# Optimization experiments

Measured on AMD Instinct MI355X. Metric: run time of the kernel, lower is better.

The kernel has to match this reference:

```python
import jax, jax.numpy as jnp
from jax import lax
import numpy as np

B = 2048; IMG = 28; K = 3; CIN = 1; HC = 32; LC = 16; WID = 64; HID = 64
LIS = IMG - 3 * (K - 1)           # 22: latent image size
FLAT = LIS * LIS * HC             # 15488
BLK = WID * LC                    # 1024: hypernet block size
T1 = 10.0; T0 = 0.0; NSTEP = 20   # fixed-step RK4 replaces adaptive dopri5
VAR = 0.1                         # p_z0 diagonal covariance


def _conv(x, w, b):  # w: [Cout,Cin,k,k], VALID conv, stride 1
    y = lax.conv_general_dilated(x, w, (1, 1), 'VALID',
                                 dimension_numbers=('NCHW', 'OIHW', 'NCHW'))
    return y + b[None, :, None, None]


def _convT(x, w, b):  # w: [Cin,Cout,k,k] (pytorch ConvTranspose2d layout)
    wf = jnp.flip(w, (2, 3)).transpose(1, 0, 2, 3)  # -> OIHW, spatially flipped
    y = lax.conv_general_dilated(x, wf, (1, 1), [(K - 1, K - 1), (K - 1, K - 1)],
                                 dimension_numbers=('NCHW', 'OIHW', 'NCHW'))
    return y + b[None, :, None, None]


def _forward(x, c0w, c0b, c1w, c1b, c2w, c2b, elw, elb, dlw, dlb,
             t0w, t0b, t1w, t1b, t2w, t2b, h1w, h1b, h2w, h2b, h3w, h3b):
    # ---- encoder (dropout in eval = identity) ----
    h = jnp.tanh(_conv(x, c0w, c0b))
    h = jnp.tanh(_conv(h, c1w, c1b))
    h = jnp.tanh(_conv(h, c2w, c2b))
    z1 = h.reshape(h.shape[0], -1) @ elw + elb          # [B, LC]
    # ---- decoder ----
    d = jnp.tanh(z1 @ dlw + dlb)                         # [B, FLAT]
    d = d.reshape(-1, HC, LIS, LIS)
    d = jnp.tanh(_convT(d, t0w, t0b))
    d = jnp.tanh(_convT(d, t1w, t1b))
    recon = _convT(d, t2w, t2b)                          # [B, CIN, 28, 28]

    # ---- CNF vector field with analytic trace ----
    def hyper(t):
        p = jnp.tanh(jnp.reshape(jnp.asarray(t, jnp.float32), (1, 1)) @ h1w + h1b)
        p = jnp.tanh(p @ h2w + h2b)
        p = (p @ h3w + h3b).reshape(-1)
        W = p[:BLK].reshape(WID, LC)
        U = p[BLK:2 * BLK].reshape(WID, LC) * jax.nn.sigmoid(p[2 * BLK:3 * BLK].reshape(WID, LC))
        Bb = p[3 * BLK:]                                 # [WID]
        return W, Bb, U

    def f(t, z):
        W, Bb, U = hyper(t)
        hh = jnp.tanh(jnp.einsum('bd,wd->wb', z, W) + Bb[:, None])   # [WID, B]
        dz = jnp.einsum('wb,wd->bd', hh, U) / WID                     # [B, LC]
        s = jnp.sum(W * U, axis=1)                                    # [WID]: sum_i W_w[i]U_w[i]
        tr = jnp.mean((1.0 - hh * hh) * s[:, None], axis=0)           # [B] analytic trace
        return dz, -tr[:, None]

    dt = (T0 - T1) / NSTEP

    def step(state, i):
        z, lp = state
        t = T1 + i * dt
        k1z, k1l = f(t, z)
        k2z, k2l = f(t + 0.5 * dt, z + 0.5 * dt * k1z)
        k3z, k3l = f(t + 0.5 * dt, z + 0.5 * dt * k2z)
        k4z, k4l = f(t + dt, z + dt * k3z)
        z = z + dt / 6.0 * (k1z + 2 * k2z + 2 * k3z + k4z)
        lp = lp + dt / 6.0 * (k1l + 2 * k2l + 2 * k3l + k4l)
        return (z, lp), None

    lp1 = jnp.zeros((z1.shape[0], 1), z1.dtype)
    (z0, lp0), _ = lax.scan(step, (z1, lp1), jnp.arange(NSTEP, dtype=jnp.float32))

    # MultivariateNormal(0, 0.1*I) log_prob
    logp = -0.5 * (LC * jnp.log(2 * jnp.pi) + LC * jnp.log(VAR) + jnp.sum(z0 * z0, -1) / VAR)
    x_probs = jnp.mean(logp - lp0[:, 0])
    return recon, x_probs


def setup_inputs() -> dict:
    key = jax.random.key(0)
    ks = jax.random.split(key, 16)
    n = jax.random.normal
    s = jnp.float32(0.05)
    z = jnp.zeros
    OUT3 = 3 * BLK + WID
    return {
        'x': n(ks[0], (B, CIN, IMG, IMG), jnp.float32),
        'c0w': n(ks[1], (HC, CIN, K, K)) * s, 'c0b': z((HC,)),
        'c1w': n(ks[2], (HC, HC, K, K)) * s, 'c1b': z((HC,)),
        'c2w': n(ks[3], (HC, HC, K, K)) * s, 'c2b': z((HC,)),
        'elw': n(ks[4], (FLAT, LC)) * s, 'elb': z((LC,)),
        'dlw': n(ks[5], (LC, FLAT)) * s, 'dlb': z((FLAT,)),
        't0w': n(ks[6], (HC, HC, K, K)) * s, 't0b': z((HC,)),
        't1w': n(ks[7], (HC, HC, K, K)) * s, 't1b': z((HC,)),
        't2w': n(ks[8], (HC, CIN, K, K)) * s, 't2b': z((CIN,)),
        'h1w': n(ks[9], (1, HID)) * s, 'h1b': z((HID,)),
        'h2w': n(ks[10], (HID, HID)) * s, 'h2b': z((HID,)),
        'h3w': n(ks[11], (HID, OUT3)) * s, 'h3b': z((OUT3,)),
    }


def reference(x, c0w, c0b, c1w, c1b, c2w, c2b, elw, elb, dlw, dlb,
              t0w, t0b, t1w, t1b, t2w, t2b, h1w, h1b, h2w, h2b, h3w, h3b):
    return _forward(x, c0w, c0b, c1w, c1b, c2w, c2b, elw, elb, dlw, dlb,
                    t0w, t0b, t1w, t1b, t2w, t2b, h1w, h1b, h2w, h2b, h3w, h3b)
```

## Files before the change

### kernel.cpp

```cpp
#include <hip/hip_runtime.h>
#include <math.h>

#define Bsz 2048

using bf16x8 = __attribute__((ext_vector_type(8))) short;
using f32x4  = __attribute__((ext_vector_type(4))) float;

__device__ __forceinline__ float fast_tanh(float x){
    float e = __expf(2.0f * x);
    return 1.0f - 2.0f / (e + 1.0f);
}
__device__ __forceinline__ float fast_sigmoid(float x){
    return 1.0f / (1.0f + __expf(-x));
}
__device__ __forceinline__ unsigned short f2b(float f){
    union { float f; unsigned u; } v; v.f = f;
    unsigned r = v.u + 0x7FFFu + ((v.u >> 16) & 1u);
    return (unsigned short)(r >> 16);
}
__device__ __forceinline__ float b2f(unsigned short s){
    union { unsigned u; float f; } v; v.u = ((unsigned)s) << 16;
    return v.f;
}

__device__ __forceinline__ float stage_t(int sidx){
    int i  = sidx >> 2, st = sidx & 3;
    float t = 10.0f - 0.5f * (float)i;
    if (st == 1 || st == 2) t -= 0.25f;
    else if (st == 3)       t -= 0.5f;
    return t;
}

__global__ void k_prep(const float* __restrict__ c1w, const float* __restrict__ c2w,
                       const float* __restrict__ t0w, const float* __restrict__ t1w,
                       const float* __restrict__ elw, const float* __restrict__ dlw,
                       const float* __restrict__ elb, const float* __restrict__ dlb,
                       const float* __restrict__ t2w,
                       unsigned short* __restrict__ wc1, unsigned short* __restrict__ wc2,
                       unsigned short* __restrict__ wt0, unsigned short* __restrict__ wt1,
                       unsigned short* __restrict__ t2wPk,
                       unsigned short* __restrict__ elwT, unsigned short* __restrict__ dlwT,
                       float* __restrict__ dlbT, float* __restrict__ z1, int full){
    int gsz = gridDim.x * 256;
    for (int i = blockIdx.x*256 + threadIdx.x; i < 9216; i += gsz){
        int ci = i & 31, co = (i >> 5) & 31, s = i >> 10;
        wc1[i] = f2b(c1w[(co*32 + ci)*9 + s]);
        wc2[i] = f2b(c2w[(co*32 + ci)*9 + s]);
        wt0[i] = f2b(t0w[(ci*32 + co)*9 + (8 - s)]);
        wt1[i] = f2b(t1w[(ci*32 + co)*9 + (8 - s)]);
    }
    if (!full) return;
    for (int i = blockIdx.x*256 + threadIdx.x; i < 288; i += gsz){
        int tap = i >> 5, ci = i & 31;
        int r = tap / 3, s = tap - r*3;
        t2wPk[i] = f2b(t2w[ci*9 + (2-r)*3 + (2-s)]);
    }
    for (int i = blockIdx.x*256 + threadIdx.x; i < 32768; i += gsz)
        z1[i] = elb[i & 15];
    for (int i = blockIdx.x*256 + threadIdx.x; i < 15488; i += gsz){
        int pos = i >> 5, ci = i & 31;
        dlbT[i] = dlb[ci*484 + pos];
    }
    for (int i = blockIdx.x*256 + threadIdx.x; i < 247808; i += gsz){
        int l = i / 15488, f2 = i - l*15488;
        int pos = f2 >> 5, ci = f2 & 31;
        elwT[i] = f2b(elw[(ci*484 + pos)*16 + l]);
    }
    for (int i = blockIdx.x*256 + threadIdx.x; i < 247808; i += gsz){
        int f2 = i >> 4, l = i & 15;
        int pos = f2 >> 5, ci = f2 & 31;
        dlwT[i] = f2b(dlw[l*15488 + ci*484 + pos]);
    }
}

__global__ void __launch_bounds__(256)
k_enc01(const float* __restrict__ x, const float* __restrict__ c0w,
        const float* __restrict__ c0b, const unsigned short* __restrict__ wc1,
        const float* __restrict__ c1b, unsigned short* __restrict__ A1,
        int cb){
    __shared__ __align__(16) unsigned short A0L[676*40];
    const int tid = threadIdx.x, b = blockIdx.x;
    const float* xin = x + (size_t)(cb + b)*784;

    for (int pos = tid; pos < 676; pos += 256){
        int y = pos / 26, xx = pos - y*26;
        float v[9];
#pragma unroll
        for (int r = 0; r < 3; r++)
#pragma unroll
            for (int s = 0; s < 3; s++)
                v[r*3+s] = xin[(y+r)*28 + xx + s];
        float acc[32];
#pragma unroll
        for (int co = 0; co < 32; co++) acc[co] = c0b[co];
#pragma unroll
        for (int k = 0; k < 9; k++)
#pragma unroll
            for (int co = 0; co < 32; co++)
                acc[co] += v[k] * c0w[co*9 + k];
        unsigned short* ob = A0L + pos*40;
#pragma unroll
        for (int g = 0; g < 8; g++){
            ushort4 o;
            o.x = f2b(fast_tanh(acc[g*4+0])); o.y = f2b(fast_tanh(acc[g*4+1]));
            o.z = f2b(fast_tanh(acc[g*4+2])); o.w = f2b(fast_tanh(acc[g*4+3]));
            *(ushort4*)(ob + g*4) = o;
        }
    }
    __syncthreads();

    const int wave = tid >> 6, lane = tid & 63;
    const int q = lane >> 4, nn = lane & 15;
    bf16x8 af[2][9];
#pragma unroll
    for (int mt = 0; mt < 2; mt++)
#pragma unroll
        for (int s = 0; s < 9; s++)
            af[mt][s] = *(const bf16x8*)(wc1 + s*1024 + (mt*16 + nn)*32 + q*8);
    float4 bc0 = *(const float4*)(c1b + q*4);
    float4 bc1 = *(const float4*)(c1b + 16 + q*4);
    unsigned short* outb = A1 + (size_t)b*25088;

    for (int t = wave; t < 36; t += 4){
        int pos = t*16 + nn;
        int oy = pos / 24, ox = pos - oy*24;
        const unsigned short* ib = A0L + (oy*26 + ox)*40 + q*8;
        f32x4 acc0 = {0.f,0.f,0.f,0.f}, acc1 = {0.f,0.f,0.f,0.f};
#pragma unroll
        for (int r = 0; r < 3; r++){
            bf16x8 b0 = *(const bf16x8*)(ib + (r*26 + 0)*40);
            bf16x8 b1 = *(const bf16x8*)(ib + (r*26 + 1)*40);
            bf16x8 b2 = *(const bf16x8*)(ib + (r*26 + 2)*40);
            acc0 = __builtin_amdgcn_mfma_f32_16x16x32_bf16(af[0][r*3+0], b0, acc0, 0,0,0);
            acc1 = __builtin_amdgcn_mfma_f32_16x16x32_bf16(af[1][r*3+0], b0, acc1, 0,0,0);
            acc0 = __builtin_amdgcn_mfma_f32_16x16x32_bf16(af[0][r*3+1], b1, acc0, 0,0,0);
            acc1 = __builtin_amdgcn_mfma_f32_16x16x32_bf16(af[1][r*3+1], b1, acc1, 0,0,0);
            acc0 = __builtin_amdgcn_mfma_f32_16x16x32_bf16(af[0][r*3+2], b2, acc0, 0,0,0);
            acc1 = __builtin_amdgcn_mfma_f32_16x16x32_bf16(af[1][r*3+2], b2, acc1, 0,0,0);
        }
        int opix = oy*24 + ox;
        ushort4 o0, o1;
        o0.x = f2b(fast_tanh(acc0[0] + bc0.x)); o0.y = f2b(fast_tanh(acc0[1] + bc0.y));
        o0.z = f2b(fast_tanh(acc0[2] + bc0.z)); o0.w = f2b(fast_tanh(acc0[3] + bc0.w));
        o1.x = f2b(fast_tanh(acc1[0] + bc1.x)); o1.y = f2b(fast_tanh(acc1[1] + bc1.y));
        o1.z = f2b(fast_tanh(acc1[2] + bc1.z)); o1.w = f2b(fast_tanh(acc1[3] + bc1.w));
        *(ushort4*)(outb + opix*32 + q*4)      = o0;
        *(ushort4*)(outb + opix*32 + 16 + q*4) = o1;
    }
}

template<int IL, int OL, int OW, int OOFF, int INS, int OUTS>
__global__ void __launch_bounds__(256)
k_convM(const unsigned short* __restrict__ in, const unsigned short* __restrict__ wg,
        const float* __restrict__ bias, unsigned short* __restrict__ out, int CH){
    constexpr int N  = OL * OL;
    constexpr int NT = (N + 15) / 16;
    const int tid = threadIdx.x;
    const int wave = tid >> 6, lane = tid & 63;
    const int q = lane >> 4, nn = lane & 15;
    const int nw = gridDim.x * 4;

    bf16x8 af[2][9];
#pragma unroll
    for (int mt = 0; mt < 2; mt++)
#pragma unroll
        for (int s = 0; s < 9; s++)
            af[mt][s] = *(const bf16x8*)(wg + s*1024 + (mt*16 + nn)*32 + q*8);
    float4 bc0 = *(const float4*)(bias + q*4);
    float4 bc1 = *(const float4*)(bias + 16 + q*4);

    for (int t = blockIdx.x*4 + wave; t < CH*NT; t += nw){
        int img = t / NT, tt = t - img*NT;
        const unsigned short* inb = in + (size_t)img * INS;
        unsigned short* outb = out + (size_t)img * OUTS;
        int pos = tt*16 + nn;
        int pc  = pos < N ? pos : N - 1;
        int oy = pc / OL, ox = pc - oy*OL;
        const unsigned short* ib = inb + (oy*IL + ox)*32 + q*8;
        f32x4 acc0 = {0.f,0.f,0.f,0.f}, acc1 = {0.f,0.f,0.f,0.f};
#pragma unroll
        for (int r = 0; r < 3; r++){
            bf16x8 b0 = *(const bf16x8*)(ib + (r*IL + 0)*32);
            bf16x8 b1 = *(const bf16x8*)(ib + (r*IL + 1)*32);
            bf16x8 b2 = *(const bf16x8*)(ib + (r*IL + 2)*32);
            acc0 = __builtin_amdgcn_mfma_f32_16x16x32_bf16(af[0][r*3+0], b0, acc0, 0,0,0);
            acc1 = __builtin_amdgcn_mfma_f32_16x16x32_bf16(af[1][r*3+0], b0, acc1, 0,0,0);
            acc0 = __builtin_amdgcn_mfma_f32_16x16x32_bf16(af[0][r*3+1], b1, acc0, 0,0,0);
            acc1 = __builtin_amdgcn_mfma_f32_16x16x32_bf16(af[1][r*3+1], b1, acc1, 0,0,0);
            acc0 = __builtin_amdgcn_mfma_f32_16x16x32_bf16(af[0][r*3+2], b2, acc0, 0,0,0);
            acc1 = __builtin_amdgcn_mfma_f32_16x16x32_bf16(af[1][r*3+2], b2, acc1, 0,0,0);
        }
        if (pos < N){
            int opix = oy*OW + ox + OOFF;
            ushort4 o0, o1;
            o0.x = f2b(fast_tanh(acc0[0] + bc0.x)); o0.y = f2b(fast_tanh(acc0[1] + bc0.y));
            o0.z = f2b(fast_tanh(acc0[2] + bc0.z)); o0.w = f2b(fast_tanh(acc0[3] + bc0.w));
            o1.x = f2b(fast_tanh(acc1[0] + bc1.x)); o1.y = f2b(fast_tanh(acc1[1] + bc1.y));
            o1.z = f2b(fast_tanh(acc1[2] + bc1.z)); o1.w = f2b(fast_tanh(acc1[3] + bc1.w));
            *(ushort4*)(outb + opix*32 + q*4)      = o0;
            *(ushort4*)(outb + opix*32 + 16 + q*4) = o1;
        }
    }
}

__global__ void __launch_bounds__(256)
k_encg(const unsigned short* __restrict__ A2, const unsigned short* __restrict__ elwT,
       float* __restrict__ z1, int cb, int CH){
    int wave = threadIdx.x >> 6, lane = threadIdx.x & 63;
    int q = lane >> 4, nn = lane & 15;
    int imgb = blockIdx.x*16;
    const unsigned short* ap = A2 + (size_t)(imgb + nn)*15488 + q*8;
    const unsigned short* bp = elwT + (size_t)nn*15488 + q*8;
    f32x4 acc = {0.f,0.f,0.f,0.f};
    int s0 = blockIdx.y*121;
#pragma unroll 2
    for (int s = s0 + wave; s < s0 + 121; s += 4){
        bf16x8 a = *(const bf16x8*)(ap + s*32);
        bf16x8 b = *(const bf16x8*)(bp + s*32);
        acc = __builtin_amdgcn_mfma_f32_16x16x32_bf16(a, b, acc, 0,0,0);
    }
    float* zp = z1 + (size_t)(cb + imgb)*16;
#pragma unroll
    for (int i = 0; i < 4; i++)
        atomicAdd(zp + (q*4 + i)*16 + nn, acc[i]);
}

__global__ void __launch_bounds__(256)
k_decgM(const float* __restrict__ z1, const unsigned short* __restrict__ dlwT,
        const float* __restrict__ dlbT, unsigned short* __restrict__ D0c, int cb){
    __shared__ float zb[16*17];
    const int tid = threadIdx.x;
    const int wave = tid >> 6, lane = tid & 63;
    const int q = lane >> 4, n = lane & 15;
    const int imgb = blockIdx.y*16;
    zb[(tid >> 4)*17 + (tid & 15)] = z1[(size_t)(cb + imgb + (tid >> 4))*16 + (tid & 15)];
    __syncthreads();

    bf16x8 zf;
    if (q < 2){
        unsigned short tmp[8];
#pragma unroll
        for (int j = 0; j < 8; j++) tmp[j] = f2b(zb[n*17 + q*8 + j]);
        zf = *(bf16x8*)tmp;
    } else {
        bf16x8 zz = {0,0,0,0,0,0,0,0}; zf = zz;
    }

#pragma unroll
    for (int ii = 0; ii < 4; ii++){
        int mt = blockIdx.x*16 + wave*4 + ii;
        if (mt >= 968) break;
        int mb = mt*16;
        bf16x8 afr;
        if (q < 2) afr = *(const bf16x8*)(dlwT + (size_t)(mb + n)*16 + q*8);
        else { bf16x8 zz = {0,0,0,0,0,0,0,0}; afr = zz; }
        f32x4 acc = {0.f,0.f,0.f,0.f};
        acc = __builtin_amdgcn_mfma_f32_16x16x32_bf16(afr, zf, acc, 0,0,0);
        float4 bias = *(const float4*)(dlbT + mb + q*4);
        ushort4 o;
        o.x = f2b(fast_tanh(acc[0] + bias.x));
        o.y = f2b(fast_tanh(acc[1] + bias.y));
        o.z = f2b(fast_tanh(acc[2] + bias.z));
        o.w = f2b(fast_tanh(acc[3] + bias.w));
        *(ushort4*)(D0c + (size_t)(imgb + n)*15488 + mb + q*4) = o;
    }
}

__global__ void __launch_bounds__(256)
k_dect0(const unsigned short* __restrict__ D0c, const unsigned short* __restrict__ wt0,
        const float* __restrict__ t0b, unsigned short* __restrict__ D1){
    __shared__ __align__(16) unsigned short D0L[676*40];
    const int tid = threadIdx.x, b = blockIdx.x;
    unsigned short* d1b = D1 + (size_t)b*25088;

    {
        uint4 zq = {0,0,0,0};
        for (int p = tid; p < 676; p += 256){
            int y = p / 26, xx = p - y*26;
            if (y < 2 || y >= 24 || xx < 2 || xx >= 24){
                uint4* pt = (uint4*)(D0L + p*40);
                pt[0] = zq; pt[1] = zq; pt[2] = zq; pt[3] = zq;
            }
        }
        for (int p = tid; p < 784; p += 256){
            int y = p / 28, xx = p - y*28;
            if (y < 2 || y >= 26 || xx < 2 || xx >= 26){
                uint4* pt = (uint4*)(d1b + p*32);
                pt[0] = zq; pt[1] = zq; pt[2] = zq; pt[3] = zq;
            }
        }
    }
    {
        const uint4* src = (const uint4*)(D0c + (size_t)b*15488);
        for (int c = tid; c < 1936; c += 256){
            uint4 v = src[c];
            int pos = c >> 2, p8 = (c & 3)*8;
            int y = pos / 22, xx = pos - y*22;
            *(uint4*)(D0L + ((y+2)*26 + xx + 2)*40 + p8) = v;
        }
    }
    __syncthreads();

    const int wave = tid >> 6, lane = tid & 63;
    const int q = lane >> 4, nn = lane & 15;
    bf16x8 af[2][9];
#pragma unroll
    for (int mt = 0; mt < 2; mt++)
#pragma unroll
        for (int s = 0; s < 9; s++)
            af[mt][s] = *(const bf16x8*)(wt0 + s*1024 + (mt*16 + nn)*32 + q*8);
    float4 bc0 = *(const float4*)(t0b + q*4);
    float4 bc1 = *(const float4*)(t0b + 16 + q*4);

    for (int t = wave; t < 36; t += 4){
        int pos = t*16 + nn;
        int oy = pos / 24, ox = pos - oy*24;
        const unsigned short* ib = D0L + (oy*26 + ox)*40 + q*8;
        f32x4 acc0 = {0.f,0.f,0.f,0.f}, acc1 = {0.f,0.f,0.f,0.f};
#pragma unroll
        for (int r = 0; r < 3; r++){
            bf16x8 b0 = *(const bf16x8*)(ib + (r*26 + 0)*40);
            bf16x8 b1 = *(const bf16x8*)(ib + (r*26 + 1)*40);
            bf16x8 b2 = *(const bf16x8*)(ib + (r*26 + 2)*40);
            acc0 = __builtin_amdgcn_mfma_f32_16x16x32_bf16(af[0][r*3+0], b0, acc0, 0,0,0);
            acc1 = __builtin_amdgcn_mfma_f32_16x16x32_bf16(af[1][r*3+0], b0, acc1, 0,0,0);
            acc0 = __builtin_amdgcn_mfma_f32_16x16x32_bf16(af[0][r*3+1], b1, acc0, 0,0,0);
            acc1 = __builtin_amdgcn_mfma_f32_16x16x32_bf16(af[1][r*3+1], b1, acc1, 0,0,0);
            acc0 = __builtin_amdgcn_mfma_f32_16x16x32_bf16(af[0][r*3+2], b2, acc0, 0,0,0);
            acc1 = __builtin_amdgcn_mfma_f32_16x16x32_bf16(af[1][r*3+2], b2, acc1, 0,0,0);
        }
        int opix = oy*28 + ox + 58;
        ushort4 o0, o1;
        o0.x = f2b(fast_tanh(acc0[0] + bc0.x)); o0.y = f2b(fast_tanh(acc0[1] + bc0.y));
        o0.z = f2b(fast_tanh(acc0[2] + bc0.z)); o0.w = f2b(fast_tanh(acc0[3] + bc0.w));
        o1.x = f2b(fast_tanh(acc1[0] + bc1.x)); o1.y = f2b(fast_tanh(acc1[1] + bc1.y));
        o1.z = f2b(fast_tanh(acc1[2] + bc1.z)); o1.w = f2b(fast_tanh(acc1[3] + bc1.w));
        *(ushort4*)(d1b + opix*32 + q*4)      = o0;
        *(ushort4*)(d1b + opix*32 + 16 + q*4) = o1;
    }
}

__global__ void __launch_bounds__(256)
k_dect12(const unsigned short* __restrict__ D1, const unsigned short* __restrict__ wt1,
         const float* __restrict__ t1b, const unsigned short* __restrict__ t2wPk,
         const float* __restrict__ t2b, float* __restrict__ out, int cb){
    __shared__ __align__(16) unsigned short D2L[900*40];
    const int tid = threadIdx.x, b = blockIdx.x;
    const unsigned short* d1b = D1 + (size_t)b*25088;
    const int wave = tid >> 6, lane = tid & 63;
    const int q = lane >> 4, nn = lane & 15;

    {
        uint4 zq = {0,0,0,0};
        for (int p = tid; p < 900; p += 256){
            int y = p / 30, xx = p - y*30;
            if (y < 2 || y >= 28 || xx < 2 || xx >= 28){
                uint4* pt = (uint4*)(D2L + p*40);
                pt[0] = zq; pt[1] = zq; pt[2] = zq; pt[3] = zq;
            }
        }
    }
    {
        bf16x8 af[2][9];
#pragma unroll
        for (int mt = 0; mt < 2; mt++)
#pragma unroll
            for (int s = 0; s < 9; s++)
                af[mt][s] = *(const bf16x8*)(wt1 + s*1024 + (mt*16 + nn)*32 + q*8);
        float4 bc0 = *(const float4*)(t1b + q*4);
        float4 bc1 = *(const float4*)(t1b + 16 + q*4);

        for (int t = wave; t < 43; t += 4){
            int pos = t*16 + nn;
            int pc  = pos < 676 ? pos : 675;
            int oy = pc / 26, ox = pc - oy*26;
            const unsigned short* ib = d1b + (oy*28 + ox)*32 + q*8;
            f32x4 acc0 = {0.f,0.f,0.f,0.f}, acc1 = {0.f,0.f,0.f,0.f};
#pragma unroll
            for (int r = 0; r < 3; r++){
                bf16x8 b0 = *(const bf16x8*)(ib + (r*28 + 0)*32);
                bf16x8 b1 = *(const bf16x8*)(ib + (r*28 + 1)*32);
                bf16x8 b2 = *(const bf16x8*)(ib + (r*28 + 2)*32);
                acc0 = __builtin_amdgcn_mfma_f32_16x16x32_bf16(af[0][r*3+0], b0, acc0, 0,0,0);
                acc1 = __builtin_amdgcn_mfma_f32_16x16x32_bf16(af[1][r*3+0], b0, acc1, 0,0,0);
                acc0 = __builtin_amdgcn_mfma_f32_16x16x32_bf16(af[0][r*3+1], b1, acc0, 0,0,0);
                acc1 = __builtin_amdgcn_mfma_f32_16x16x32_bf16(af[1][r*3+1], b1, acc1, 0,0,0);
                acc0 = __builtin_amdgcn_mfma_f32_16x16x32_bf16(af[0][r*3+2], b2, acc0, 0,0,0);
                acc1 = __builtin_amdgcn_mfma_f32_16x16x32_bf16(af[1][r*3+2], b2, acc1, 0,0,0);
            }
            if (pos < 676){
                int opix = (oy + 2)*30 + ox + 2;
                ushort4 o0, o1;
                o0.x = f2b(fast_tanh(acc0[0] + bc0.x)); o0.y = f2b(fast_tanh(acc0[1] + bc0.y));
                o0.z = f2b(fast_tanh(acc0[2] + bc0.z)); o0.w = f2b(fast_tanh(acc0[3] + bc0.w));
                o1.x = f2b(fast_tanh(acc1[0] + bc1.x)); o1.y = f2b(fast_tanh(acc1[1] + bc1.y));
                o1.z = f2b(fast_tanh(acc1[2] + bc1.z)); o1.w = f2b(fast_tanh(acc1[3] + bc1.w));
                *(ushort4*)(D2L + opix*40 + q*4)      = o0;
                *(ushort4*)(D2L + opix*40 + 16 + q*4) = o1;
            }
        }
    }
    __syncthreads();

    {
        bf16x8 wf[9];
#pragma unroll
        for (int tap = 0; tap < 9; tap++)
            wf[tap] = *(const bf16x8*)(t2wPk + tap*32 + q*8);
        float t2b0 = t2b[0];
        for (int t = wave; t < 49; t += 4){
            int p = t*16 + nn;
            int y = p / 28, xx = p - y*28;
            const unsigned short* bbase = D2L + (y*30 + xx)*40 + q*8;
            f32x4 acc = {0.f,0.f,0.f,0.f};
#pragma unroll
            for (int r = 0; r < 3; r++){
                acc = __builtin_amdgcn_mfma_f32_16x16x32_bf16(wf[r*3+0],
                        *(const bf16x8*)(bbase + (r*30 + 0)*40), acc, 0,0,0);
                acc = __builtin_amdgcn_mfma_f32_16x16x32_bf16(wf[r*3+1],
                        *(const bf16x8*)(bbase + (r*30 + 1)*40), acc, 0,0,0);
                acc = __builtin_amdgcn_mfma_f32_16x16x32_bf16(wf[r*3+2],
                        *(const bf16x8*)(bbase + (r*30 + 2)*40), acc, 0,0,0);
            }
            if (q == 0)
                out[(size_t)(cb + b)*784 + p] = acc[0] + t2b0;
        }
    }
}

template<int LOUT, int INW, int OUTW, int OUTOFF>
// ... 209 lines not shown
        ushort4 o0 = {0,0,0,0}, o1 = {0,0,0,0};
        if (q < 2){
            const float* wp = p3 + (c*16 + m)*16 + q*8;
            o0.x = f2b(wp[0]); o0.y = f2b(wp[1]); o0.z = f2b(wp[2]); o0.w = f2b(wp[3]);
            o1.x = f2b(wp[4]); o1.y = f2b(wp[5]); o1.z = f2b(wp[6]); o1.w = f2b(wp[7]);
        }
        *(ushort4*)(gW + tid*8)     = o0;
        *(ushort4*)(gW + tid*8 + 4) = o1;
    }
    if (tid < 128){
        int lane = tid & 63, kb = tid >> 6;
        int q = lane >> 4, d = lane & 15;
        unsigned short uo[8];
#pragma unroll
        for (int j = 0; j < 8; j++){
            int w = kb*32 + q*8 + j;
            float u = p3[1024 + w*16 + d] * fast_sigmoid(p3[2048 + w*16 + d]);
            uo[j] = f2b(u);
        }
        *(ushort4*)(gU + tid*8)     = *(ushort4*)&uo[0];
        *(ushort4*)(gU + tid*8 + 4) = *(ushort4*)&uo[4];
    } else if (tid < 192){
        int w = tid - 128;
        g[1536 + w] = p3[3072 + w];
    } else {
        int w = tid - 192;
        float s = 0.f;
#pragma unroll
        for (int d = 0; d < 16; d++){
            float u = p3[1024 + w*16 + d] * fast_sigmoid(p3[2048 + w*16 + d]);
            s += p3[w*16 + d] * u;
        }
        g[1600 + w] = s;
        sred[w] = s;
    }
    __syncthreads();
    if (tid == 0){
        float st = 0.f;
#pragma unroll
        for (int w = 0; w < 64; w++) st += sred[w];
        g[1664] = st;
    }
}

__global__ void k_hyper(const float* __restrict__ h1w, const float* __restrict__ h1b,
                        const float* __restrict__ h2w, const float* __restrict__ h2b,
                        const float* __restrict__ h3w, const float* __restrict__ h3b,
                        float* __restrict__ hyp){
    int sidx = blockIdx.x;
    float t = stage_t(sidx);
    __shared__ float p1[64], p2[64];
    __shared__ float p3[3136];
    int tid = threadIdx.x;
    if (tid < 64) p1[tid] = fast_tanh(t * h1w[tid] + h1b[tid]);
    __syncthreads();
    if (tid < 64){
        float a = h2b[tid];
#pragma unroll
        for (int k = 0; k < 64; k++) a += p1[k] * h2w[k*64 + tid];
        p2[tid] = fast_tanh(a);
    }
    __syncthreads();
    for (int m = tid; m < 3136; m += 256){
        float a = h3b[m];
#pragma unroll
        for (int k = 0; k < 64; k++) a += p2[k] * h3w[k*3136 + m];
        p3[m] = a;
    }
    __syncthreads();
    float* g = hyp + (size_t)sidx * 2304;
    for (int m = tid; m < 1024; m += 256){
        g[m] = p3[m];
        float u = p3[1024 + m] * fast_sigmoid(p3[2048 + m]);
        g[1024 + (m & 15)*64 + (m >> 4)] = u;
        p3[1024 + m] = u;
    }
    if (tid < 64) g[2048 + tid] = p3[3072 + tid];
    __syncthreads();
    if (tid < 64){
        float s = 0.f;
#pragma unroll
        for (int d = 0; d < 16; d++) s += p3[tid*16 + d] * p3[1024 + tid*16 + d];
        g[2112 + tid] = s;
    }
}

struct PM {
    bf16x8 Wf[4];
    bf16x8 Uf[2];
    float4 Bbf[4];
    float4 sf[4];
    float stot;
};
__device__ __forceinline__ void loadPM(const float* __restrict__ g, int lane, int q, PM& p){
    const unsigned short* gW = (const unsigned short*)g;
    const unsigned short* gU = (const unsigned short*)(g + 1024);
#pragma unroll
    for (int c = 0; c < 4; c++)
        p.Wf[c] = *(const bf16x8*)(gW + (c*64 + lane)*8);
#pragma unroll
    for (int kb = 0; kb < 2; kb++)
        p.Uf[kb] = *(const bf16x8*)(gU + (kb*64 + lane)*8);
#pragma unroll
    for (int c = 0; c < 4; c++){
        p.Bbf[c] = *(const float4*)(g + 1536 + c*16 + q*4);
        p.sf[c]  = *(const float4*)(g + 1600 + c*16 + q*4);
    }
    p.stot = g[1664];
}

__global__ void __launch_bounds__(64)
k_cnfM(const float* __restrict__ z1, const float* __restrict__ hyp,
       float* __restrict__ part){
    __shared__ __align__(16) unsigned short zsb[16*24];
    __shared__ __align__(16) unsigned short hhT[16*72];
    const int lane = threadIdx.x;
    const int q = lane >> 4, d = lane & 15;
    const float dt = -0.5f;

    float z[4], zacc[4], lacc[4], lp[4];
#pragma unroll
    for (int i = 0; i < 4; i++){
        z[i] = z1[(size_t)(blockIdx.x*16 + q*4 + i)*16 + d];
        zacc[i] = 0.f; lacc[i] = 0.f; lp[i] = 0.f;
        zsb[(q*4 + i)*24 + d] = f2b(z[i]);
    }
    PM pm0, pm1;
    loadPM(hyp, lane, q, pm0);

#pragma unroll 2
    for (int sidx = 0; sidx < 80; sidx++){
        PM& cur = (sidx & 1) ? pm1 : pm0;
        PM& nxt = (sidx & 1) ? pm0 : pm1;
        if (sidx < 79) loadPM(hyp + (size_t)(sidx + 1)*2048, lane, q, nxt);

        bf16x8 zb;
        if (q < 2) zb = *(const bf16x8*)(zsb + d*24 + q*8);
        else { bf16x8 zz2 = {0,0,0,0,0,0,0,0}; zb = zz2; }

        f32x4 h0 = {0,0,0,0}, h1 = {0,0,0,0}, h2 = {0,0,0,0}, h3 = {0,0,0,0};
        h0 = __builtin_amdgcn_mfma_f32_16x16x32_bf16(cur.Wf[0], zb, h0, 0,0,0);
        h1 = __builtin_amdgcn_mfma_f32_16x16x32_bf16(cur.Wf[1], zb, h1, 0,0,0);
        h2 = __builtin_amdgcn_mfma_f32_16x16x32_bf16(cur.Wf[2], zb, h2, 0,0,0);
        h3 = __builtin_amdgcn_mfma_f32_16x16x32_bf16(cur.Wf[3], zb, h3, 0,0,0);

        float partial = 0.f;
        f32x4 hc[4] = {h0, h1, h2, h3};
#pragma unroll
        for (int c = 0; c < 4; c++){
            ushort4 o;
            float t0 = fast_tanh(hc[c][0] + cur.Bbf[c].x);
            float t1 = fast_tanh(hc[c][1] + cur.Bbf[c].y);
            float t2 = fast_tanh(hc[c][2] + cur.Bbf[c].z);
            float t3 = fast_tanh(hc[c][3] + cur.Bbf[c].w);
            partial += t0*t0*cur.sf[c].x + t1*t1*cur.sf[c].y
                     + t2*t2*cur.sf[c].z + t3*t3*cur.sf[c].w;
            o.x = f2b(t0); o.y = f2b(t1); o.z = f2b(t2); o.w = f2b(t3);
            *(ushort4*)(hhT + d*72 + c*16 + q*4) = o;
        }
        partial += __shfl_xor(partial, 16);
        partial += __shfl_xor(partial, 32);
        float trFull = (cur.stot - partial) * (1.f/64.f);

        bf16x8 a20 = *(const bf16x8*)(hhT + d*72 + q*8);
        bf16x8 a21 = *(const bf16x8*)(hhT + d*72 + 32 + q*8);
        f32x4 dzac = {0,0,0,0};
        dzac = __builtin_amdgcn_mfma_f32_16x16x32_bf16(a20, cur.Uf[0], dzac, 0,0,0);
        dzac = __builtin_amdgcn_mfma_f32_16x16x32_bf16(a21, cur.Uf[1], dzac, 0,0,0);

        int st = sidx & 3;
        float wgt = (st == 0 || st == 3) ? 1.f : 2.f;
#pragma unroll
        for (int i = 0; i < 4; i++){
            float dz = dzac[i] * (1.f/64.f);
            float dl = -__shfl(trFull, q*4 + i);
            zacc[i] += wgt * dz;
            lacc[i] += wgt * dl;
            float zsv;
            if (st < 3){
                float aa = (st == 2) ? 1.0f : 0.5f;
                zsv = z[i] + aa * dt * dz;
            } else {
                z[i]  += (dt/6.f) * zacc[i];
                lp[i] += (dt/6.f) * lacc[i];
                zsv = z[i];
                zacc[i] = 0.f; lacc[i] = 0.f;
            }
            zsb[(q*4 + i)*24 + d] = f2b(zsv);
        }
    }
    float sq[4];
#pragma unroll
    for (int i = 0; i < 4; i++) sq[i] = z[i]*z[i];
#pragma unroll
    for (int off = 1; off < 16; off <<= 1){
#pragma unroll
        for (int i = 0; i < 4; i++) sq[i] += __shfl_xor(sq[i], off, 16);
    }
    if (d == 0){
#pragma unroll
        for (int i = 0; i < 4; i++){
            float logp = -0.5f * (16.f*1.8378770664093453f
                                 + 16.f*(-2.302585092994046f) + sq[i]*10.f);
            part[blockIdx.x*16 + q*4 + i] = logp - lp[i];
        }
    }
}

struct PF { float4 Wr[4]; float4 Ur[4]; float Bb, sw; };
__device__ __forceinline__ void load_pf(const float* __restrict__ g,
                                        int lane, int q, int d, PF& p){
    const float4* w4 = (const float4*)(g + lane*16);
    p.Wr[0] = w4[0]; p.Wr[1] = w4[1]; p.Wr[2] = w4[2]; p.Wr[3] = w4[3];
    const float4* u4 = (const float4*)(g + 1024 + d*64 + q*16);
    p.Ur[0] = u4[0]; p.Ur[1] = u4[1]; p.Ur[2] = u4[2]; p.Ur[3] = u4[3];
    p.Bb = g[2048 + lane];
    p.sw = g[2112 + lane];
}
__global__ void __launch_bounds__(64)
k_cnf_f(const float* __restrict__ z1, const float* __restrict__ hyp,
        float* __restrict__ part){
    __shared__ __align__(16) float zsl[16];
    __shared__ __align__(16) float hhl[64];
    const int lane = threadIdx.x;
    const int q = lane >> 4, d = lane & 15;
    const float dt = -0.5f;
    float z  = z1[(size_t)blockIdx.x*16 + d];
    float zs = z;
    float lp = 0.f, zacc = 0.f, lacc = 0.f;
    if (lane < 16) zsl[lane] = zs;
    PF cur, nxt;
    load_pf(hyp, lane, q, d, cur);
    for (int sidx = 0; sidx < 80; sidx++){
        __syncthreads();
        if (sidx < 79) load_pf(hyp + (size_t)(sidx + 1)*2304, lane, q, d, nxt);
        const float4* zp = (const float4*)zsl;
        float4 z0 = zp[0], z1v = zp[1], z2 = zp[2], z3 = zp[3];
        float a = cur.Bb;
        a += z0.x*cur.Wr[0].x + z0.y*cur.Wr[0].y + z0.z*cur.Wr[0].z + z0.w*cur.Wr[0].w;
        a += z1v.x*cur.Wr[1].x + z1v.y*cur.Wr[1].y + z1v.z*cur.Wr[1].z + z1v.w*cur.Wr[1].w;
        a += z2.x*cur.Wr[2].x + z2.y*cur.Wr[2].y + z2.z*cur.Wr[2].z + z2.w*cur.Wr[2].w;
        a += z3.x*cur.Wr[3].x + z3.y*cur.Wr[3].y + z3.z*cur.Wr[3].z + z3.w*cur.Wr[3].w;
        float hh = fast_tanh(a);
        float e = (1.f - hh*hh) * cur.sw;
#pragma unroll
        for (int off = 1; off < 64; off <<= 1)
            e += __shfl_xor(e, off);
        hhl[lane] = hh;
        __syncthreads();
        const float4* hp = (const float4*)(hhl + q*16);
        float4 h0 = hp[0], h1 = hp[1], h2 = hp[2], h3 = hp[3];
        float dzp = 0.f;
        dzp += h0.x*cur.Ur[0].x + h0.y*cur.Ur[0].y + h0.z*cur.Ur[0].z + h0.w*cur.Ur[0].w;
        dzp += h1.x*cur.Ur[1].x + h1.y*cur.Ur[1].y + h1.z*cur.Ur[1].z + h1.w*cur.Ur[1].w;
        dzp += h2.x*cur.Ur[2].x + h2.y*cur.Ur[2].y + h2.z*cur.Ur[2].z + h2.w*cur.Ur[2].w;
        dzp += h3.x*cur.Ur[3].x + h3.y*cur.Ur[3].y + h3.z*cur.Ur[3].z + h3.w*cur.Ur[3].w;
        dzp += __shfl_xor(dzp, 16);
        dzp += __shfl_xor(dzp, 32);
        float dz = dzp * (1.f/64.f);
        float dl = -e  * (1.f/64.f);
        int st = sidx & 3;
        float wgt = (st == 0 || st == 3) ? 1.f : 2.f;
        zacc += wgt * dz;
        lacc += wgt * dl;
        if (st < 3){
            float aa = (st == 2) ? 1.0f : 0.5f;
            zs = z + aa * dt * dz;
        } else {
            z  += (dt/6.f) * zacc;
            lp += (dt/6.f) * lacc;
            zs = z;
            zacc = 0.f; lacc = 0.f;
        }
        if (lane < 16) zsl[lane] = zs;
        cur = nxt;
    }
    float sq = z * z;
#pragma unroll
    for (int off = 1; off < 16; off <<= 1) sq += __shfl_xor(sq, off, 16);
    float logp = -0.5f * (16.f*1.8378770664093453f + 16.f*(-2.302585092994046f) + sq*10.f);
    if (lane == 0) part[blockIdx.x] = logp - lp;
}

__global__ void k_final(const float* __restrict__ part, float* __restrict__ out){
    __shared__ float red[256];
    int tid = threadIdx.x;
    float s = 0.f;
#pragma unroll
// ... 1 lines not shown
    red[tid] = s;
    __syncthreads();
    for (int st = 128; st > 0; st >>= 1){
        if (tid < st) red[tid] += red[tid + st];
        __syncthreads();
    }
    if (tid == 0) out[1605632] = red[0] * (1.f/2048.f);
}

extern "C" void kernel_launch(void* const* d_in, const int* in_sizes, int n_in,
                              void* d_out, int out_size, void* d_ws, size_t ws_size,
                              hipStream_t stream){
    const float* x   = (const float*)d_in[0];
    const float* c0w = (const float*)d_in[1];
    const float* c0b = (const float*)d_in[2];
    const float* c1w = (const float*)d_in[3];
    const float* c1b = (const float*)d_in[4];
    const float* c2w = (const float*)d_in[5];
    const float* c2b = (const float*)d_in[6];
    const float* elw = (const float*)d_in[7];
    const float* elb = (const float*)d_in[8];
    const float* dlw = (const float*)d_in[9];
    const float* dlb = (const float*)d_in[10];
    const float* t0w = (const float*)d_in[11];
    const float* t0b = (const float*)d_in[12];
    const float* t1w = (const float*)d_in[13];
    const float* t1b = (const float*)d_in[14];
    const float* t2w = (const float*)d_in[15];
    const float* t2b = (const float*)d_in[16];
    const float* h1w = (const float*)d_in[17];
    const float* h1b = (const float*)d_in[18];
    const float* h2w = (const float*)d_in[19];
    const float* h2b = (const float*)d_in[20];
    const float* h3w = (const float*)d_in[21];
    const float* h3b = (const float*)d_in[22];

    float* ws   = (float*)d_ws;
    float* z1   = ws;
    float* hyp  = z1 + 32768;
    float* part = hyp + 184320;
    float* p2ws = part + 2048;
    float* p3ws = p2ws + 5120;
    float* dlbT = p3ws + 256000;
    unsigned short* wc1  = (unsigned short*)(dlbT + 15488);
    unsigned short* wc2  = wc1 + 9216;
    unsigned short* wt0  = wc2 + 9216;
    unsigned short* wt1  = wt0 + 9216;
    unsigned short* t2wPk = wt1 + 9216;
    unsigned short* elwT = t2wPk + 288;
    unsigned short* dlwT = elwT + 247808;
    unsigned short* act  = dlwT + 247808;
    float* rec  = (float*)d_out;

    const size_t MISC = 3048512;
    int CH = 0;
    const int cands[6] = {2048, 1024, 512, 256, 128, 64};
    for (int c = 0; c < 6; c++){
        size_t need = MISC + (size_t)cands[c] * 81152;
        if (need <= ws_size){ CH = cands[c]; break; }
    }

    if (CH == 0){
        k_hyper<<<80, 256, 0, stream>>>(h1w, h1b, h2w, h2b, h3w, h3b, hyp);
        k_prep <<<64,   256, 0, stream>>>(c1w, c2w, t0w, t1w, elw, dlw, elb, dlb, t2w,
                                          wc1, wc2, wt0, wt1, t2wPk, wt1, wt1, z1, z1, 0);
        k_enc_f<<<2048, 256, 0, stream>>>(x, c0w, c0b, wc1, c1b, wc2, c2b, elw, elb, z1);
        k_cnf_f<<<2048,  64, 0, stream>>>(z1, hyp, part);
        k_dec_f<<<2048, 256, 0, stream>>>(z1, dlw, dlb, wt0, t0b, wt1, t1b, t2w, t2b, rec);
        k_final<<<1,    256, 0, stream>>>(part, rec);
        return;
    }

    k_hyp1<<<80,           64, 0, stream>>>(h1w, h1b, h2w, h2b, p2ws);
    k_hyp2<<<dim3(13,80), 256, 0, stream>>>(p2ws, h3w, h3b, p3ws);
    k_hyp3<<<80,          256, 0, stream>>>(p3ws, hyp);

    k_prep<<<64, 256, 0, stream>>>(c1w, c2w, t0w, t1w, elw, dlw, elb, dlb, t2w,
                                   wc1, wc2, wt0, wt1, t2wPk, elwT, dlwT, dlbT, z1, 1);

    unsigned short* X = act;
    unsigned short* Y = X + (size_t)CH*25088;

    for (int cb = 0; cb < Bsz; cb += CH){
        k_enc01<<<CH, 256, 0, stream>>>(x, c0w, c0b, wc1, c1b, X, cb);
        k_convM<24,22,22,0, 25088, 15488><<<(CH*31 + 15)/16, 256, 0, stream>>>(X, wc2, c2b, Y, CH);
        k_encg<<<dim3(CH/16, 4), 256, 0, stream>>>(Y, elwT, z1, cb, CH);
        k_decgM<<<dim3(61, CH/16), 256, 0, stream>>>(z1, dlwT, dlbT, Y, cb);
        k_dect0<<<CH, 256, 0, stream>>>(Y, wt0, t0b, X);
        k_dect12<<<CH, 256, 0, stream>>>(X, wt1, t1b, t2wPk, t2b, rec, cb);
    }
    k_cnfM <<<128,  64, 0, stream>>>(z1, hyp, part);
    k_final<<<1,   256, 0, stream>>>(part, rec);
}
```

Measured before the change: 583.7 us.

## Fold CNF integration and final reduction into decoder kernels; shrink LDS pitch

The CNF RK4 integration, previously its own 128-block launch after the batch loop, now runs as extra blocks of the last chunk's transposed-conv kernel. Its long serial 80-step latency can then overlap decoder work instead of running alone at the end. The final log-likelihood reduction likewise becomes an extra block of the last k_dect12 launch, which removes two kernel launches. The LDS row pitch for the conv staging buffers drops from 40 to 36 elements to cut shared memory use and change the bank mapping. The catch is that 16-byte vector accesses now sit at 72-byte strides that are not 16-byte aligned.

```diff
diff --git a/kernel.cpp b/kernel.cpp
--- a/kernel.cpp
+++ b/kernel.cpp
@@ -78,7 +78,7 @@
         const float* __restrict__ c0b, const unsigned short* __restrict__ wc1,
         const float* __restrict__ c1b, unsigned short* __restrict__ A1,
         int cb){
-    __shared__ __align__(16) unsigned short A0L[676*40];
+    __shared__ __align__(16) unsigned short A0L[676*36];
     const int tid = threadIdx.x, b = blockIdx.x;
     const float* xin = x + (size_t)(cb + b)*784;
 
@@ -98,7 +98,7 @@
 #pragma unroll
             for (int co = 0; co < 32; co++)
                 acc[co] += v[k] * c0w[co*9 + k];
-        unsigned short* ob = A0L + pos*40;
+        unsigned short* ob = A0L + pos*36;
 #pragma unroll
         for (int g = 0; g < 8; g++){
             ushort4 o;
@@ -124,13 +124,13 @@
     for (int t = wave; t < 36; t += 4){
         int pos = t*16 + nn;
         int oy = pos / 24, ox = pos - oy*24;
-        const unsigned short* ib = A0L + (oy*26 + ox)*40 + q*8;
+        const unsigned short* ib = A0L + (oy*26 + ox)*36 + q*8;
         f32x4 acc0 = {0.f,0.f,0.f,0.f}, acc1 = {0.f,0.f,0.f,0.f};
 #pragma unroll
         for (int r = 0; r < 3; r++){
-            bf16x8 b0 = *(const bf16x8*)(ib + (r*26 + 0)*40);
-            bf16x8 b1 = *(const bf16x8*)(ib + (r*26 + 1)*40);
-            bf16x8 b2 = *(const bf16x8*)(ib + (r*26 + 2)*40);
+            bf16x8 b0 = *(const bf16x8*)(ib + (r*26 + 0)*36);
+            bf16x8 b1 = *(const bf16x8*)(ib + (r*26 + 1)*36);
+            bf16x8 b2 = *(const bf16x8*)(ib + (r*26 + 2)*36);
             acc0 = __builtin_amdgcn_mfma_f32_16x16x32_bf16(af[0][r*3+0], b0, acc0, 0,0,0);
             acc1 = __builtin_amdgcn_mfma_f32_16x16x32_bf16(af[1][r*3+0], b0, acc1, 0,0,0);
             acc0 = __builtin_amdgcn_mfma_f32_16x16x32_bf16(af[0][r*3+1], b1, acc0, 0,0,0);
@@ -266,19 +266,149 @@
     }
 }
 
+struct PM {
+    bf16x8 Wf[4];
+    bf16x8 Uf[2];
+    float4 Bbf[4];
+    float4 sf[4];
+    float stot;
+};
+__device__ __forceinline__ void loadPM(const float* __restrict__ g, int lane, int q, PM& p){
+    const unsigned short* gW = (const unsigned short*)g;
+    const unsigned short* gU = (const unsigned short*)(g + 1024);
+#pragma unroll
+    for (int c = 0; c < 4; c++)
+        p.Wf[c] = *(const bf16x8*)(gW + (c*64 + lane)*8);
+#pragma unroll
+    for (int kb = 0; kb < 2; kb++)
+        p.Uf[kb] = *(const bf16x8*)(gU + (kb*64 + lane)*8);
+#pragma unroll
+    for (int c = 0; c < 4; c++){
+        p.Bbf[c] = *(const float4*)(g + 1536 + c*16 + q*4);
+        p.sf[c]  = *(const float4*)(g + 1600 + c*16 + q*4);
+    }
+    p.stot = g[1664];
+}
+
+__device__ __forceinline__ void cnf_body(const float* __restrict__ z1,
+                                         const float* __restrict__ hyp,
+                                         float* __restrict__ part, int bid,
+                                         unsigned short* zsb, unsigned short* hhT){
+    const int lane = threadIdx.x;
+    const int q = lane >> 4, d = lane & 15;
+    const float dt = -0.5f;
+
+    float z[4], zacc[4], lacc[4], lp[4];
+#pragma unroll
+    for (int i = 0; i < 4; i++){
+        z[i] = z1[(size_t)(bid*16 + q*4 + i)*16 + d];
+        zacc[i] = 0.f; lacc[i] = 0.f; lp[i] = 0.f;
+        zsb[(q*4 + i)*24 + d] = f2b(z[i]);
+    }
+    PM pm0, pm1;
+    loadPM(hyp, lane, q, pm0);
+
+#pragma unroll 2
+    for (int sidx = 0; sidx < 80; sidx++){
+        PM& cur = (sidx & 1) ? pm1 : pm0;
+        PM& nxt = (sidx & 1) ? pm0 : pm1;
+        if (sidx < 79) loadPM(hyp + (size_t)(sidx + 1)*2048, lane, q, nxt);
+
+        bf16x8 zb;
+        if (q < 2) zb = *(const bf16x8*)(zsb + d*24 + q*8);
+        else { bf16x8 zz2 = {0,0,0,0,0,0,0,0}; zb = zz2; }
+
+        f32x4 h0 = {0,0,0,0}, h1 = {0,0,0,0}, h2 = {0,0,0,0}, h3 = {0,0,0,0};
+        h0 = __builtin_amdgcn_mfma_f32_16x16x32_bf16(cur.Wf[0], zb, h0, 0,0,0);
+        h1 = __builtin_amdgcn_mfma_f32_16x16x32_bf16(cur.Wf[1], zb, h1, 0,0,0);
+        h2 = __builtin_amdgcn_mfma_f32_16x16x32_bf16(cur.Wf[2], zb, h2, 0,0,0);
+        h3 = __builtin_amdgcn_mfma_f32_16x16x32_bf16(cur.Wf[3], zb, h3, 0,0,0);
+
+        float partial = 0.f;
+        f32x4 hc[4] = {h0, h1, h2, h3};
+#pragma unroll
+        for (int c = 0; c < 4; c++){
+            ushort4 o;
+            float t0 = fast_tanh(hc[c][0] + cur.Bbf[c].x);
+            float t1 = fast_tanh(hc[c][1] + cur.Bbf[c].y);
+            float t2 = fast_tanh(hc[c][2] + cur.Bbf[c].z);
+            float t3 = fast_tanh(hc[c][3] + cur.Bbf[c].w);
+            partial += t0*t0*cur.sf[c].x + t1*t1*cur.sf[c].y
+                     + t2*t2*cur.sf[c].z + t3*t3*cur.sf[c].w;
+            o.x = f2b(t0); o.y = f2b(t1); o.z = f2b(t2); o.w = f2b(t3);
+            *(ushort4*)(hhT + d*72 + c*16 + q*4) = o;
+        }
+        partial += __shfl_xor(partial, 16);
+        partial += __shfl_xor(partial, 32);
+        float trFull = (cur.stot - partial) * (1.f/64.f);
+
+        bf16x8 a20 = *(const bf16x8*)(hhT + d*72 + q*8);
+        bf16x8 a21 = *(const bf16x8*)(hhT + d*72 + 32 + q*8);
+        f32x4 dzac = {0,0,0,0};
+        dzac = __builtin_amdgcn_mfma_f32_16x16x32_bf16(a20, cur.Uf[0], dzac, 0,0,0);
+        dzac = __builtin_amdgcn_mfma_f32_16x16x32_bf16(a21, cur.Uf[1], dzac, 0,0,0);
+
+        int st = sidx & 3;
+        float wgt = (st == 0 || st == 3) ? 1.f : 2.f;
+#pragma unroll
+        for (int i = 0; i < 4; i++){
+            float dz = dzac[i] * (1.f/64.f);
+            float dl = -__shfl(trFull, q*4 + i);
+            zacc[i] += wgt * dz;
+            lacc[i] += wgt * dl;
+            float zsv;
+            if (st < 3){
+                float aa = (st == 2) ? 1.0f : 0.5f;
+                zsv = z[i] + aa * dt * dz;
+            } else {
+                z[i]  += (dt/6.f) * zacc[i];
+                lp[i] += (dt/6.f) * lacc[i];
+                zsv = z[i];
+                zacc[i] = 0.f; lacc[i] = 0.f;
+            }
+            zsb[(q*4 + i)*24 + d] = f2b(zsv);
+        }
+    }
+    float sq[4];
+#pragma unroll
+    for (int i = 0; i < 4; i++) sq[i] = z[i]*z[i];
+#pragma unroll
+    for (int off = 1; off < 16; off <<= 1){
+#pragma unroll
+        for (int i = 0; i < 4; i++) sq[i] += __shfl_xor(sq[i], off, 16);
+    }
+    if (d == 0){
+#pragma unroll
+        for (int i = 0; i < 4; i++){
+            float logp = -0.5f * (16.f*1.8378770664093453f
+                                 + 16.f*(-2.302585092994046f) + sq[i]*10.f);
+            part[bid*16 + q*4 + i] = logp - lp[i];
+        }
+    }
+}
+
 __global__ void __launch_bounds__(256)
-k_dect0(const unsigned short* __restrict__ D0c, const unsigned short* __restrict__ wt0,
-        const float* __restrict__ t0b, unsigned short* __restrict__ D1){
-    __shared__ __align__(16) unsigned short D0L[676*40];
+k_dect0c(const unsigned short* __restrict__ D0c, const unsigned short* __restrict__ wt0,
+         const float* __restrict__ t0b, unsigned short* __restrict__ D1,
+         const float* __restrict__ z1, const float* __restrict__ hyp,
+         float* __restrict__ part, int CH){
+    __shared__ __align__(16) unsigned short D0L[676*36];
+    __shared__ __align__(16) unsigned short zsbS[16*24];
+    __shared__ __align__(16) unsigned short hhTS[16*72];
     const int tid = threadIdx.x, b = blockIdx.x;
+
+    if (b >= CH){
+        if (tid >= 64) return;
+        cnf_body(z1, hyp, part, b - CH, zsbS, hhTS);
+        return;
+    }
     unsigned short* d1b = D1 + (size_t)b*25088;
-
     {
         uint4 zq = {0,0,0,0};
         for (int p = tid; p < 676; p += 256){
             int y = p / 26, xx = p - y*26;
             if (y < 2 || y >= 24 || xx < 2 || xx >= 24){
-                uint4* pt = (uint4*)(D0L + p*40);
+                uint4* pt = (uint4*)(D0L + p*36);
                 pt[0] = zq; pt[1] = zq; pt[2] = zq; pt[3] = zq;
             }
         }
@@ -296,7 +426,7 @@
             uint4 v = src[c];
             int pos = c >> 2, p8 = (c & 3)*8;
             int y = pos / 22, xx = pos - y*22;
-            *(uint4*)(D0L + ((y+2)*26 + xx + 2)*40 + p8) = v;
+            *(uint4*)(D0L + ((y+2)*26 + xx + 2)*36 + p8) = v;
         }
     }
     __syncthreads();
@@ -315,13 +445,13 @@
     for (int t = wave; t < 36; t += 4){
         int pos = t*16 + nn;
         int oy = pos / 24, ox = pos - oy*24;
-        const unsigned short* ib = D0L + (oy*26 + ox)*40 + q*8;
+        const unsigned short* ib = D0L + (oy*26 + ox)*36 + q*8;
         f32x4 acc0 = {0.f,0.f,0.f,0.f}, acc1 = {0.f,0.f,0.f,0.f};
 #pragma unroll
         for (int r = 0; r < 3; r++){
-            bf16x8 b0 = *(const bf16x8*)(ib + (r*26 + 0)*40);
-            bf16x8 b1 = *(const bf16x8*)(ib + (r*26 + 1)*40);
-            bf16x8 b2 = *(const bf16x8*)(ib + (r*26 + 2)*40);
+            bf16x8 b0 = *(const bf16x8*)(ib + (r*26 + 0)*36);
+            bf16x8 b1 = *(const bf16x8*)(ib + (r*26 + 1)*36);
+            bf16x8 b2 = *(const bf16x8*)(ib + (r*26 + 2)*36);
             acc0 = __builtin_amdgcn_mfma_f32_16x16x32_bf16(af[0][r*3+0], b0, acc0, 0,0,0);
             acc1 = __builtin_amdgcn_mfma_f32_16x16x32_bf16(af[1][r*3+0], b0, acc1, 0,0,0);
             acc0 = __builtin_amdgcn_mfma_f32_16x16x32_bf16(af[0][r*3+1], b1, acc0, 0,0,0);
@@ -343,9 +473,24 @@
 __global__ void __launch_bounds__(256)
 k_dect12(const unsigned short* __restrict__ D1, const unsigned short* __restrict__ wt1,
          const float* __restrict__ t1b, const unsigned short* __restrict__ t2wPk,
-         const float* __restrict__ t2b, float* __restrict__ out, int cb){
+         const float* __restrict__ t2b, float* __restrict__ out,
+         const float* __restrict__ part, int cb, int CH){
     __shared__ __align__(16) unsigned short D2L[900*40];
     const int tid = threadIdx.x, b = blockIdx.x;
+    if (b >= CH){
+        __shared__ float red[256];
+        float s = 0.f;
+#pragma unroll
+        for (int k = 0; k < 8; k++) s += part[tid + k*256];
+        red[tid] = s;
+        __syncthreads();
+        for (int st = 128; st > 0; st >>= 1){
+            if (tid < st) red[tid] += red[tid + st];
+            __syncthreads();
+        }
+        if (tid == 0) out[1605632] = red[0] * (1.f/2048.f);
+        return;
+    }
     const unsigned short* d1b = D1 + (size_t)b*25088;
     const int wave = tid >> 6, lane = tid & 63;
     const int q = lane >> 4, nn = lane & 15;
@@ -721,128 +866,6 @@
 #pragma unroll
         for (int d = 0; d < 16; d++) s += p3[tid*16 + d] * p3[1024 + tid*16 + d];
         g[2112 + tid] = s;
-    }
-}
-
-struct PM {
-    bf16x8 Wf[4];
-    bf16x8 Uf[2];
-    float4 Bbf[4];
-    float4 sf[4];
-    float stot;
-};
-__device__ __forceinline__ void loadPM(const float* __restrict__ g, int lane, int q, PM& p){
-    const unsigned short* gW = (const unsigned short*)g;
-    const unsigned short* gU = (const unsigned short*)(g + 1024);
-#pragma unroll
-    for (int c = 0; c < 4; c++)
-        p.Wf[c] = *(const bf16x8*)(gW + (c*64 + lane)*8);
-#pragma unroll
-    for (int kb = 0; kb < 2; kb++)
-        p.Uf[kb] = *(const bf16x8*)(gU + (kb*64 + lane)*8);
-#pragma unroll
-    for (int c = 0; c < 4; c++){
-        p.Bbf[c] = *(const float4*)(g + 1536 + c*16 + q*4);
-        p.sf[c]  = *(const float4*)(g + 1600 + c*16 + q*4);
-    }
-    p.stot = g[1664];
-}
-
-__global__ void __launch_bounds__(64)
-k_cnfM(const float* __restrict__ z1, const float* __restrict__ hyp,
-       float* __restrict__ part){
-    __shared__ __align__(16) unsigned short zsb[16*24];
-    __shared__ __align__(16) unsigned short hhT[16*72];
-    const int lane = threadIdx.x;
-    const int q = lane >> 4, d = lane & 15;
-    const float dt = -0.5f;
-
-    float z[4], zacc[4], lacc[4], lp[4];
-#pragma unroll
-    for (int i = 0; i < 4; i++){
-        z[i] = z1[(size_t)(blockIdx.x*16 + q*4 + i)*16 + d];
-        zacc[i] = 0.f; lacc[i] = 0.f; lp[i] = 0.f;
-        zsb[(q*4 + i)*24 + d] = f2b(z[i]);
-    }
-    PM pm0, pm1;
-    loadPM(hyp, lane, q, pm0);
-
-#pragma unroll 2
-    for (int sidx = 0; sidx < 80; sidx++){
-        PM& cur = (sidx & 1) ? pm1 : pm0;
-        PM& nxt = (sidx & 1) ? pm0 : pm1;
-        if (sidx < 79) loadPM(hyp + (size_t)(sidx + 1)*2048, lane, q, nxt);
-
-        bf16x8 zb;
-        if (q < 2) zb = *(const bf16x8*)(zsb + d*24 + q*8);
-        else { bf16x8 zz2 = {0,0,0,0,0,0,0,0}; zb = zz2; }
-
-        f32x4 h0 = {0,0,0,0}, h1 = {0,0,0,0}, h2 = {0,0,0,0}, h3 = {0,0,0,0};
-        h0 = __builtin_amdgcn_mfma_f32_16x16x32_bf16(cur.Wf[0], zb, h0, 0,0,0);
-        h1 = __builtin_amdgcn_mfma_f32_16x16x32_bf16(cur.Wf[1], zb, h1, 0,0,0);
-        h2 = __builtin_amdgcn_mfma_f32_16x16x32_bf16(cur.Wf[2], zb, h2, 0,0,0);
-        h3 = __builtin_amdgcn_mfma_f32_16x16x32_bf16(cur.Wf[3], zb, h3, 0,0,0);
-
-        float partial = 0.f;
-        f32x4 hc[4] = {h0, h1, h2, h3};
-#pragma unroll
-        for (int c = 0; c < 4; c++){
-            ushort4 o;
-            float t0 = fast_tanh(hc[c][0] + cur.Bbf[c].x);
-            float t1 = fast_tanh(hc[c][1] + cur.Bbf[c].y);
-            float t2 = fast_tanh(hc[c][2] + cur.Bbf[c].z);
-            float t3 = fast_tanh(hc[c][3] + cur.Bbf[c].w);
-            partial += t0*t0*cur.sf[c].x + t1*t1*cur.sf[c].y
-                     + t2*t2*cur.sf[c].z + t3*t3*cur.sf[c].w;
-            o.x = f2b(t0); o.y = f2b(t1); o.z = f2b(t2); o.w = f2b(t3);
-            *(ushort4*)(hhT + d*72 + c*16 + q*4) = o;
-        }
-        partial += __shfl_xor(partial, 16);
-        partial += __shfl_xor(partial, 32);
-        float trFull = (cur.stot - partial) * (1.f/64.f);
-
-        bf16x8 a20 = *(const bf16x8*)(hhT + d*72 + q*8);
-        bf16x8 a21 = *(const bf16x8*)(hhT + d*72 + 32 + q*8);
-        f32x4 dzac = {0,0,0,0};
-        dzac = __builtin_amdgcn_mfma_f32_16x16x32_bf16(a20, cur.Uf[0], dzac, 0,0,0);
-        dzac = __builtin_amdgcn_mfma_f32_16x16x32_bf16(a21, cur.Uf[1], dzac, 0,0,0);
-
-        int st = sidx & 3;
-        float wgt = (st == 0 || st == 3) ? 1.f : 2.f;
-#pragma unroll
-        for (int i = 0; i < 4; i++){
-            float dz = dzac[i] * (1.f/64.f);
-            float dl = -__shfl(trFull, q*4 + i);
-            zacc[i] += wgt * dz;
-            lacc[i] += wgt * dl;
-            float zsv;
-            if (st < 3){
-                float aa = (st == 2) ? 1.0f : 0.5f;
-                zsv = z[i] + aa * dt * dz;
-            } else {
-                z[i]  += (dt/6.f) * zacc[i];
-                lp[i] += (dt/6.f) * lacc[i];
-                zsv = z[i];
-                zacc[i] = 0.f; lacc[i] = 0.f;
-            }
-            zsb[(q*4 + i)*24 + d] = f2b(zsv);
-        }
-    }
-    float sq[4];
-#pragma unroll
-    for (int i = 0; i < 4; i++) sq[i] = z[i]*z[i];
-#pragma unroll
-    for (int off = 1; off < 16; off <<= 1){
-#pragma unroll
-        for (int i = 0; i < 4; i++) sq[i] += __shfl_xor(sq[i], off, 16);
-    }
-    if (d == 0){
-#pragma unroll
-        for (int i = 0; i < 4; i++){
-            float logp = -0.5f * (16.f*1.8378770664093453f
-                                 + 16.f*(-2.302585092994046f) + sq[i]*10.f);
-            part[blockIdx.x*16 + q*4 + i] = logp - lp[i];
-        }
     }
 }
 
@@ -1010,13 +1033,12 @@
     unsigned short* Y = X + (size_t)CH*25088;
 
     for (int cb = 0; cb < Bsz; cb += CH){
+        int last = (cb + CH >= Bsz);
         k_enc01<<<CH, 256, 0, stream>>>(x, c0w, c0b, wc1, c1b, X, cb);
         k_convM<24,22,22,0, 25088, 15488><<<(CH*31 + 15)/16, 256, 0, stream>>>(X, wc2, c2b, Y, CH);
         k_encg<<<dim3(CH/16, 4), 256, 0, stream>>>(Y, elwT, z1, cb, CH);
         k_decgM<<<dim3(61, CH/16), 256, 0, stream>>>(z1, dlwT, dlbT, Y, cb);
-        k_dect0<<<CH, 256, 0, stream>>>(Y, wt0, t0b, X);
-        k_dect12<<<CH, 256, 0, stream>>>(X, wt1, t1b, t2wPk, t2b, rec, cb);
-    }
-    k_cnfM <<<128,  64, 0, stream>>>(z1, hyp, part);
-    k_final<<<1,   256, 0, stream>>>(part, rec);
-}
+        k_dect0c<<<CH + (last ? 128 : 0), 256, 0, stream>>>(Y, wt0, t0b, X, z1, hyp, part, CH);
+        k_dect12<<<CH + (last ? 1 : 0), 256, 0, stream>>>(X, wt1, t1b, t2wPk, t2b, rec, part, cb, CH);
+    }
+}
```

Result: slower. 625.1 us (+7.1%).
